# Kernel tuning notes

Measured on AMD Instinct MI355X. Metric: run time of the kernel, lower is better.

## Reference

```python
import jax, jax.numpy as jnp
import numpy as np

NUM_EXPERTS = 64
GROUP_SIZE = 4
NUM_GROUPS = NUM_EXPERTS // GROUP_SIZE  # 16
TOP_K = 2
B, S, D = 8, 4096, 2048


def setup_inputs() -> dict:
    key = jax.random.key(0)
    k1, k2, k3 = jax.random.split(key, 3)
    x = jax.random.normal(k1, (B, S, D), dtype=jnp.float32)
    # nn.Linear weight layout [out, in], init std=0.001
    Wg = jax.random.normal(k2, (NUM_GROUPS, D), dtype=jnp.float32) * 0.001
    We = jax.random.normal(k3, (GROUP_SIZE, D), dtype=jnp.float32) * 0.001
    return {"x": x, "Wg": Wg, "We": We}


def reference(x, Wg, We):
    b, s, d = x.shape
    n_tok = b * s
    x_flat = x.reshape(n_tok, d)

    # Stage 1: group routing (top-1 group)
    group_logits = x_flat @ Wg.T                      # [N, G]
    group_probs = jax.nn.softmax(group_logits, axis=-1)
    top_gw, top_gi = jax.lax.top_k(group_probs, 1)    # [N, 1]
    chosen_group = top_gi[:, 0]                        # [N] int
    chosen_group_w = top_gw[:, 0]                      # [N]

    # Stage 2: local expert routing (top-k within group)
    local_logits = x_flat @ We.T                       # [N, group_size]
    local_probs = jax.nn.softmax(local_logits, axis=-1)
    expert_offset = chosen_group * GROUP_SIZE          # [N]
    top_lw, top_li = jax.lax.top_k(local_probs, TOP_K) # [N, k]
    top_expert_idx = expert_offset[:, None] + top_li   # [N, k]

    top_lw = top_lw / (jnp.sum(top_lw, axis=-1, keepdims=True) + 1e-7)
    final_weights = chosen_group_w[:, None] * top_lw   # [N, k]

    # Dispatch mask: scatter final_weights at chosen expert columns.
    # top-k local indices are distinct, so set (== torch scatter_) is safe.
    rows = jnp.arange(n_tok)[:, None]
    dispatch_mask = jnp.zeros((n_tok, NUM_EXPERTS), dtype=x.dtype)
    dispatch_mask = dispatch_mask.at[rows, top_expert_idx].set(final_weights)

    # Auxiliary losses
    expert_load = dispatch_mask.sum(axis=0)            # [E]
    target_load = expert_load.sum() / NUM_EXPERTS
    load_balance_loss = jnp.mean((expert_load - target_load) ** 2)
    z_loss = jnp.mean(group_logits ** 2) + jnp.mean(local_logits ** 2)
    router_loss = 0.001 * (load_balance_loss + z_loss)

    return jax.lax.stop_gradient(final_weights), dispatch_mask, router_loss
```

## Files before the change

### kernel.cpp

```cpp
#include <hip/hip_runtime.h>


#define NTOK    32768
#define DIM     2048
#define NG      16
#define GS      4
#define NE      64
#define NR      20
#define DC      256
#define NCHUNK  (DIM / DC)
#define TPB     256
#define TPW     4
#define TPBK    16
#define NSHADOW 32

typedef float f4 __attribute__((ext_vector_type(4)));

__device__ __forceinline__ f4 ldnt(const float* p) {
    return __builtin_nontemporal_load((const f4*)p);
}

__global__ __launch_bounds__(TPB, 2) void router_main(
    const float* __restrict__ x,
    const float* __restrict__ Wg,
    const float* __restrict__ We,
    float* __restrict__ fw_out,
    float* __restrict__ dm_out,
    float* __restrict__ ws)
{
    __shared__ float lds_load[NE];
    __shared__ float lds_z;

    const int tid  = threadIdx.x;
    const int lane = tid & 63;
    const int wave = tid >> 6;
    const long t_base = (long)blockIdx.x * TPBK + wave * TPW;

    if (tid < NE) lds_load[tid] = 0.0f;
    if (tid == 0) lds_z = 0.0f;
    __syncthreads();

    float acc[TPW][NR];
    #pragma unroll
    for (int t = 0; t < TPW; ++t)
        #pragma unroll
        for (int r = 0; r < NR; ++r) acc[t][r] = 0.0f;

    f4 xa[TPW], xb[TPW];
    #pragma unroll
    for (int t = 0; t < TPW; ++t)
        xa[t] = ldnt(x + (size_t)(t_base + t) * DIM + lane * 4);

    #pragma unroll 1
    for (int c = 0; c < NCHUNK; c += 2) {
        #pragma unroll
        for (int t = 0; t < TPW; ++t)
            xb[t] = ldnt(x + (size_t)(t_base + t) * DIM + (c + 1) * DC + lane * 4);

        #pragma unroll
        for (int r = 0; r < NR; ++r) {
            const float* wp = (r < NG) ? (Wg + (size_t)r * DIM)
                                       : (We + (size_t)(r - NG) * DIM);
            f4 w = *(const f4*)(wp + c * DC + lane * 4);
            #pragma unroll
            for (int t = 0; t < TPW; ++t) {
                acc[t][r] += xa[t].x * w.x + xa[t].y * w.y
                           + xa[t].z * w.z + xa[t].w * w.w;
            }
        }

        if (c + 2 < NCHUNK) {
            #pragma unroll
            for (int t = 0; t < TPW; ++t)
                xa[t] = ldnt(x + (size_t)(t_base + t) * DIM + (c + 2) * DC + lane * 4);
        }

        #pragma unroll
        for (int r = 0; r < NR; ++r) {
            const float* wp = (r < NG) ? (Wg + (size_t)r * DIM)
                                       : (We + (size_t)(r - NG) * DIM);
            f4 w = *(const f4*)(wp + (c + 1) * DC + lane * 4);
            #pragma unroll
            for (int t = 0; t < TPW; ++t) {
                acc[t][r] += xb[t].x * w.x + xb[t].y * w.y
                           + xb[t].z * w.z + xb[t].w * w.w;
            }
        }
    }

    #pragma unroll
    for (int t = 0; t < TPW; ++t)
        #pragma unroll
        for (int r = 0; r < NR; ++r) {
            float v = acc[t][r];
            #pragma unroll
            for (int s = 32; s > 0; s >>= 1) v += __shfl_xor(v, s, 64);
            acc[t][r] = v;
        }

    #pragma unroll
    for (int t = 0; t < TPW; ++t) {
        float m16 = acc[t][0];
        #pragma unroll
        for (int r = 1; r < NG; ++r) m16 = fmaxf(m16, acc[t][r]);
        float den = 0.0f, bm = -1.0f; int gi = 0;
        #pragma unroll
        for (int r = 0; r < NG; ++r) {
            float e = expf(acc[t][r] - m16);
            den += e;
            if (e > bm) { bm = e; gi = r; }
        }
        float gw = bm / den;

        float m4 = fmaxf(fmaxf(acc[t][NG + 0], acc[t][NG + 1]),
                         fmaxf(acc[t][NG + 2], acc[t][NG + 3]));
        float pr[GS]; float s4 = 0.0f;
        #pragma unroll
        for (int r = 0; r < GS; ++r) { pr[r] = expf(acc[t][NG + r] - m4); s4 += pr[r]; }
        float inv4 = 1.0f / s4;
        #pragma unroll
        for (int r = 0; r < GS; ++r) pr[r] *= inv4;

        int i0 = 0; float v0 = pr[0];
        #pragma unroll
        for (int r = 1; r < GS; ++r) if (pr[r] > v0) { v0 = pr[r]; i0 = r; }
        int i1 = -1; float v1 = -1.0f;
        #pragma unroll
        for (int r = 0; r < GS; ++r) if (r != i0 && pr[r] > v1) { v1 = pr[r]; i1 = r; }

        float nrm = v0 + v1 + 1e-7f;
        float sf0 = gw * (v0 / nrm);
        float sf1 = gw * (v1 / nrm);
        int   se0 = (gi << 2) + i0;
        int   se1 = (gi << 2) + i1;

        float sg = 0.0f;
        #pragma unroll
        for (int r = 0; r < NG; ++r) sg += acc[t][r] * acc[t][r];
        float sl = 0.0f;
        #pragma unroll
        for (int r = 0; r < GS; ++r) sl += acc[t][NG + r] * acc[t][NG + r];
        float sz = sg * (1.0f / 16.0f) + sl * 0.25f;

        const long tok = t_base + t;
        if (lane < 16) {
            int col4 = lane * 4;
            float4 v;
            v.x = (col4 + 0 == se0) ? sf0 : (col4 + 0 == se1) ? sf1 : 0.0f;
            v.y = (col4 + 1 == se0) ? sf0 : (col4 + 1 == se1) ? sf1 : 0.0f;
            v.z = (col4 + 2 == se0) ? sf0 : (col4 + 2 == se1) ? sf1 : 0.0f;
            v.w = (col4 + 3 == se0) ? sf0 : (col4 + 3 == se1) ? sf1 : 0.0f;
            *(float4*)(dm_out + (size_t)tok * NE + col4) = v;
        } else if (lane == 16) {
            *(float2*)(fw_out + tok * 2) = make_float2(sf0, sf1);
        } else if (lane == 17) {
            atomicAdd(&lds_load[se0], sf0);
        } else if (lane == 18) {
            atomicAdd(&lds_load[se1], sf1);
        } else if (lane == 19) {
            atomicAdd(&lds_z, sz);
        }
    }

    __syncthreads();
    if (tid < NE) atomicAdd(&ws[(blockIdx.x & (NSHADOW - 1)) * NE + tid], lds_load[tid]);
    if (tid == 0) atomicAdd(&ws[NSHADOW * NE], lds_z);
}

__global__ void router_finalize(const float* __restrict__ ws, float* __restrict__ out_loss)
{
    int e = threadIdx.x;
    float load = 0.0f;
    #pragma unroll
    for (int s = 0; s < NSHADOW; ++s) load += ws[s * NE + e];
    float tot = load;
    #pragma unroll
    for (int s = 32; s > 0; s >>= 1) tot += __shfl_xor(tot, s, 64);
    float target = tot * (1.0f / NE);
    float dev = load - target;
    float sq = dev * dev;
    #pragma unroll
    for (int s = 32; s > 0; s >>= 1) sq += __shfl_xor(sq, s, 64);
    if (e == 0) {
        float lb = sq * (1.0f / NE);
        float z  = ws[NSHADOW * NE] * (1.0f / NTOK);
        out_loss[0] = 0.001f * (lb + z);
    }
}

extern "C" void kernel_launch(void* const* d_in, const int* in_sizes, int n_in,
                              void* d_out, int out_size, void* d_ws, size_t ws_size,
                              hipStream_t stream)
{
    const float* x  = (const float*)d_in[0];
    const float* Wg = (const float*)d_in[1];
    const float* We = (const float*)d_in[2];
    float* out = (float*)d_out;
    float* fw  = out;
    float* dm  = out + (size_t)NTOK * 2;
    float* ls  = out + (size_t)NTOK * 2 + (size_t)NTOK * NE;
    float* ws  = (float*)d_ws;

    hipMemsetAsync(ws, 0, (NSHADOW * NE + 1) * sizeof(float), stream);
    router_main<<<NTOK / TPBK, TPB, 0, stream>>>(x, Wg, We, fw, dm, ws);
    router_finalize<<<1, 64, 0, stream>>>(ws, ls);
}
```

Baseline: 429.3 us.

## Stage router weight chunks in LDS via double-buffered global_load_lds

```diff
diff --git a/kernel.cpp b/kernel.cpp
--- a/kernel.cpp
+++ b/kernel.cpp
@@ -12,6 +12,7 @@
 #define TPB     256
 #define TPW     4
 #define TPBK    16
+#define WCH     (NR * DC)
 #define NSHADOW 32
 
 typedef float f4 __attribute__((ext_vector_type(4)));
@@ -20,7 +21,14 @@
     return __builtin_nontemporal_load((const f4*)p);
 }
 
-__global__ __launch_bounds__(TPB, 2) void router_main(
+__device__ __forceinline__ void gl_lds16(const float* g, float* l) {
+    __builtin_amdgcn_global_load_lds(
+        (const __attribute__((address_space(1))) void*)g,
+        (__attribute__((address_space(3))) void*)l,
+        16, 0, 0);
+}
+
+__global__ __launch_bounds__(TPB, 3) void router_main(
     const float* __restrict__ x,
     const float* __restrict__ Wg,
     const float* __restrict__ We,
@@ -28,6 +36,7 @@
     float* __restrict__ dm_out,
     float* __restrict__ ws)
 {
+    __shared__ float wbuf[2][WCH];
     __shared__ float lds_load[NE];
     __shared__ float lds_z;
 
@@ -38,54 +47,67 @@
 
     if (tid < NE) lds_load[tid] = 0.0f;
     if (tid == 0) lds_z = 0.0f;
+
+    const float* wg_l = Wg + lane * 4;
+    const float* we_l = We + lane * 4;
+    auto stage_w = [&](int c, float* dst) {
+        #pragma unroll
+        for (int k = 0; k < 4; ++k) {
+            const int r = k * 4 + wave;
+            gl_lds16(wg_l + (size_t)r * DIM + c * DC, dst + r * DC);
+        }
+        gl_lds16(we_l + (size_t)wave * DIM + c * DC, dst + (NG + wave) * DC);
+    };
+
+    float acc[TPW][NR];
+    #pragma unroll
+    for (int t = 0; t < TPW; ++t)
+        #pragma unroll
+        for (int r = 0; r < NR; ++r) acc[t][r] = 0.0f;
+
+    const float* xp = x + (size_t)t_base * DIM + lane * 4;
+
+    stage_w(0, &wbuf[0][0]);
+    f4 xa[TPW], xb[TPW];
+    #pragma unroll
+    for (int t = 0; t < TPW; ++t) xa[t] = ldnt(xp + (size_t)t * DIM);
     __syncthreads();
-
-    float acc[TPW][NR];
-    #pragma unroll
-    for (int t = 0; t < TPW; ++t)
-        #pragma unroll
-        for (int r = 0; r < NR; ++r) acc[t][r] = 0.0f;
-
-    f4 xa[TPW], xb[TPW];
-    #pragma unroll
-    for (int t = 0; t < TPW; ++t)
-        xa[t] = ldnt(x + (size_t)(t_base + t) * DIM + lane * 4);
 
     #pragma unroll 1
     for (int c = 0; c < NCHUNK; c += 2) {
+        stage_w(c + 1, &wbuf[1][0]);
         #pragma unroll
         for (int t = 0; t < TPW; ++t)
-            xb[t] = ldnt(x + (size_t)(t_base + t) * DIM + (c + 1) * DC + lane * 4);
+            xb[t] = ldnt(xp + (size_t)t * DIM + (c + 1) * DC);
 
         #pragma unroll
         for (int r = 0; r < NR; ++r) {
-            const float* wp = (r < NG) ? (Wg + (size_t)r * DIM)
-                                       : (We + (size_t)(r - NG) * DIM);
-            f4 w = *(const f4*)(wp + c * DC + lane * 4);
+            f4 w = *(const f4*)(&wbuf[0][r * DC + lane * 4]);
             #pragma unroll
             for (int t = 0; t < TPW; ++t) {
                 acc[t][r] += xa[t].x * w.x + xa[t].y * w.y
                            + xa[t].z * w.z + xa[t].w * w.w;
             }
         }
+        __syncthreads();
 
         if (c + 2 < NCHUNK) {
+            stage_w(c + 2, &wbuf[0][0]);
             #pragma unroll
             for (int t = 0; t < TPW; ++t)
-                xa[t] = ldnt(x + (size_t)(t_base + t) * DIM + (c + 2) * DC + lane * 4);
+                xa[t] = ldnt(xp + (size_t)t * DIM + (c + 2) * DC);
         }
 
         #pragma unroll
         for (int r = 0; r < NR; ++r) {
-            const float* wp = (r < NG) ? (Wg + (size_t)r * DIM)
-                                       : (We + (size_t)(r - NG) * DIM);
-            f4 w = *(const f4*)(wp + (c + 1) * DC + lane * 4);
+            f4 w = *(const f4*)(&wbuf[1][r * DC + lane * 4]);
             #pragma unroll
             for (int t = 0; t < TPW; ++t) {
                 acc[t][r] += xb[t].x * w.x + xb[t].y * w.y
                            + xb[t].z * w.z + xb[t].w * w.w;
             }
         }
+        __syncthreads();
     }
 
     #pragma unroll
```

After: 583.6 us. 1.36x slower.
